# Kernel optimization log

Hardware: AMD Instinct MI355X
Metric: run time of the kernel (lower is better)

## Reference

```python
import jax, jax.numpy as jnp
import numpy as np

B, C, H, W = 2, 3, 96, 96
OC = 2  # conv output channels
EPS = 1e-5

def setup_inputs() -> dict:
    key = jax.random.key(0)
    k1, k2, k3, k4 = jax.random.split(key, 4)
    return {
        "X_tnext": jax.random.normal(k1, (B, C, H, W), dtype=jnp.float32),
        "X_hat_tnext": jax.random.normal(k2, (B, C, H, W), dtype=jnp.float32),
        "conv_w": jax.random.normal(k3, (OC, C, 3, 3), dtype=jnp.float32) * 0.1,
        "conv_b": jax.random.normal(k4, (OC,), dtype=jnp.float32) * 0.1,
        "gamma": jnp.ones((OC,), dtype=jnp.float32),
        "beta": jnp.zeros((OC,), dtype=jnp.float32),
    }

def reference(X_tnext, X_hat_tnext, conv_w, conv_b, gamma, beta):
    b, c, h, w = X_tnext.shape
    n = h * w
    q = X_tnext.reshape(b, c, n)
    k = X_hat_tnext.reshape(b, c, n)
    # corr4D: [b, n, n] = q^T k / sqrt(c)  (materialized O(N^2) volume, as in source)
    corr = jnp.einsum('bcn,bcm->bnm', q, k) / jnp.sqrt(jnp.asarray(c, jnp.float32))
    # weighted aggregation: corr @ X_tnext (broadcast over channels)
    agg = jnp.einsum('bnm,bcm->bcn', corr, q).reshape(b, c, h, w)
    # Conv2d(3->2, k=3, s=1, p=1)
    y = jax.lax.conv_general_dilated(
        agg, conv_w, window_strides=(1, 1), padding='SAME',
        dimension_numbers=('NCHW', 'OIHW', 'NCHW'))
    y = y + conv_b[None, :, None, None]
    # BatchNorm2d (training-mode batch statistics, biased var, eps=1e-5)
    mean = jnp.mean(y, axis=(0, 2, 3), keepdims=True)
    var = jnp.var(y, axis=(0, 2, 3), keepdims=True)
    y = (y - mean) * jax.lax.rsqrt(var + EPS)
    y = y * gamma[None, :, None, None] + beta[None, :, None, None]
    # LeakyReLU(0.1)
    return jnp.where(y >= 0, y, 0.1 * y)
```

## Files before the change

kernel.cpp:

```cpp
#include <hip/hip_runtime.h>
#include <math.h>

namespace {
constexpr int kB = 2, kC = 3, kOC = 2, kH = 96, kW = 96;
constexpr int kN   = kH * kW;
constexpr int kPix = kB * kOC * kN;
constexpr float kEps   = 1e-5f;
constexpr float kScale = 0.57735026918962576f;

constexpr int WS_M   = 0;
constexpr int WS_SUM = 24;
constexpr int WS_SQ  = 26;
constexpr int WS_Y   = 32;
}

__global__ void k1_corr(const float* __restrict__ q, const float* __restrict__ kk,
                        float* __restrict__ ws) {
    const int idx = blockIdx.x;
    const int b   = idx / 9;
    const int cp  = (idx % 9) / 3;
    const int c   = idx % 3;
    const float* kp = kk + (size_t)(b * kC + cp) * kN;
    const float* qp = q  + (size_t)(b * kC + c ) * kN;
    float part = 0.f;
    for (int n = threadIdx.x; n < kN; n += 256)
        part += kp[n] * qp[n];
    __shared__ float red[256];
    red[threadIdx.x] = part;
    __syncthreads();
    for (int s = 128; s > 0; s >>= 1) {
        if (threadIdx.x < s) red[threadIdx.x] += red[threadIdx.x + s];
        __syncthreads();
    }
    if (threadIdx.x == 0) {
        ws[WS_M + idx] = red[0];
        if (idx == 0) {
            ws[WS_SUM + 0] = 0.f; ws[WS_SUM + 1] = 0.f;
            ws[WS_SQ  + 0] = 0.f; ws[WS_SQ  + 1] = 0.f;
        }
    }
}

__global__ void k2_conv(const float* __restrict__ q, const float* __restrict__ cw,
                        const float* __restrict__ cb, float* __restrict__ ws) {
    const int plane = blockIdx.x / 36;
    const int b   = plane / kOC;
    const int oc  = plane % kOC;
    const int pix = (blockIdx.x % 36) * 256 + threadIdx.x;
    const int h = pix / kW, w = pix % kW;

    __shared__ float sM[9];
    __shared__ float sW[kC * 9];
    if (threadIdx.x < 9) sM[threadIdx.x] = ws[WS_M + b * 9 + threadIdx.x];
    if (threadIdx.x >= 64 && threadIdx.x < 64 + kC * 9)
        sW[threadIdx.x - 64] = cw[oc * kC * 9 + (threadIdx.x - 64)];
    __syncthreads();

    const float* qb = q + (size_t)b * kC * kN;
    float acc = cb[oc];
    #pragma unroll
    for (int dh = 0; dh < 3; ++dh) {
        const int hh = h + dh - 1;
        if (hh < 0 || hh >= kH) continue;
        #pragma unroll
        for (int dw = 0; dw < 3; ++dw) {
            const int ww = w + dw - 1;
            if (ww < 0 || ww >= kW) continue;
            const int p = hh * kW + ww;
            const float q0 = qb[p];
            const float q1 = qb[kN + p];
            const float q2 = qb[2 * kN + p];
            #pragma unroll
            for (int ic = 0; ic < kC; ++ic) {
                const float a = kScale * (sM[0 * 3 + ic] * q0 +
                                          sM[1 * 3 + ic] * q1 +
                                          sM[2 * 3 + ic] * q2);
                acc += a * sW[ic * 9 + dh * 3 + dw];
            }
        }
    }
    ws[WS_Y + plane * kN + pix] = acc;

    __shared__ float rs[256], rq[256];
    rs[threadIdx.x] = acc;
    rq[threadIdx.x] = acc * acc;
    __syncthreads();
    for (int s = 128; s > 0; s >>= 1) {
        if (threadIdx.x < s) {
            rs[threadIdx.x] += rs[threadIdx.x + s];
            rq[threadIdx.x] += rq[threadIdx.x + s];
        }
        __syncthreads();
    }
    if (threadIdx.x == 0) {
        atomicAdd(&ws[WS_SUM + oc], rs[0]);
        atomicAdd(&ws[WS_SQ  + oc], rq[0]);
    }
}

__global__ void k3_bn(const float* __restrict__ ws, const float* __restrict__ gamma,
                      const float* __restrict__ beta, float* __restrict__ out) {
    const int i  = blockIdx.x * 256 + threadIdx.x;
    const int oc = (i / kN) % kOC;
    const float inv  = 1.f / (float)(kB * kN);
    const float mean = ws[WS_SUM + oc] * inv;
    const float var  = ws[WS_SQ + oc] * inv - mean * mean;
    const float rstd = rsqrtf(var + kEps);
    float y = (ws[WS_Y + i] - mean) * rstd * gamma[oc] + beta[oc];
    out[i] = (y >= 0.f) ? y : 0.1f * y;
}

extern "C" void kernel_launch(void* const* d_in, const int* in_sizes, int n_in,
                              void* d_out, int out_size, void* d_ws, size_t ws_size,
                              hipStream_t stream) {
    const float* X      = (const float*)d_in[0];
    const float* Xhat   = (const float*)d_in[1];
    const float* conv_w = (const float*)d_in[2];
    const float* conv_b = (const float*)d_in[3];
    const float* gamma  = (const float*)d_in[4];
    const float* beta   = (const float*)d_in[5];
    float* out = (float*)d_out;
    float* ws  = (float*)d_ws;

    k1_corr<<<kB * kC * kC, 256, 0, stream>>>(X, Xhat, ws);
    k2_conv<<<kPix / 256, 256, 0, stream>>>(X, conv_w, conv_b, ws);
    k3_bn  <<<kPix / 256, 256, 0, stream>>>(ws, gamma, beta, out);
}
```

Baseline: 83.04 us.

## Fuse correlation, conv and batchnorm into one kernel with grid barrier

Merges the three kernels into one launch. Each block recomputes the 3x3 channel correlation matrix itself, using warp shuffles instead of a separate reduction kernel, then runs the convolution. Blocks publish per-block partial sums and spin on a global atomic counter until all have arrived, then reduce the batchnorm statistics and write the output directly, so the intermediate Y buffer is never written or re-read. The barrier assumes all 144 blocks are resident at once. It also relies on the workspace counter being set to a poison value before each call so the first block can reset it, which depends on harness behaviour. Every block also repeats the correlation reads, trading redundant work for fewer launches.

```diff
diff --git a/kernel.cpp b/kernel.cpp
--- a/kernel.cpp
+++ b/kernel.cpp
@@ -3,60 +3,64 @@
 
 namespace {
 constexpr int kB = 2, kC = 3, kOC = 2, kH = 96, kW = 96;
-constexpr int kN   = kH * kW;
-constexpr int kPix = kB * kOC * kN;
+constexpr int kN      = kH * kW;
+constexpr int kChunks = kN / 256;
+constexpr int kBlocks = kB * kOC * kChunks;
 constexpr float kEps   = 1e-5f;
 constexpr float kScale = 0.57735026918962576f;
-
-constexpr int WS_M   = 0;
-constexpr int WS_SUM = 24;
-constexpr int WS_SQ  = 26;
-constexpr int WS_Y   = 32;
+constexpr unsigned kPoison = 0xAAAAAAAAu;
 }
 
-__global__ void k1_corr(const float* __restrict__ q, const float* __restrict__ kk,
-                        float* __restrict__ ws) {
-    const int idx = blockIdx.x;
-    const int b   = idx / 9;
-    const int cp  = (idx % 9) / 3;
-    const int c   = idx % 3;
-    const float* kp = kk + (size_t)(b * kC + cp) * kN;
-    const float* qp = q  + (size_t)(b * kC + c ) * kN;
-    float part = 0.f;
-    for (int n = threadIdx.x; n < kN; n += 256)
-        part += kp[n] * qp[n];
-    __shared__ float red[256];
-    red[threadIdx.x] = part;
-    __syncthreads();
-    for (int s = 128; s > 0; s >>= 1) {
-        if (threadIdx.x < s) red[threadIdx.x] += red[threadIdx.x + s];
-        __syncthreads();
-    }
-    if (threadIdx.x == 0) {
-        ws[WS_M + idx] = red[0];
-        if (idx == 0) {
-            ws[WS_SUM + 0] = 0.f; ws[WS_SUM + 1] = 0.f;
-            ws[WS_SQ  + 0] = 0.f; ws[WS_SQ  + 1] = 0.f;
-        }
-    }
-}
+__global__ __launch_bounds__(256) void fused_fea(
+    const float* __restrict__ X,    const float* __restrict__ Xhat,
+    const float* __restrict__ cw,   const float* __restrict__ cb,
+    const float* __restrict__ gamma,const float* __restrict__ beta,
+    float* __restrict__ out, unsigned* __restrict__ wsu) {
 
-__global__ void k2_conv(const float* __restrict__ q, const float* __restrict__ cw,
-                        const float* __restrict__ cb, float* __restrict__ ws) {
-    const int plane = blockIdx.x / 36;
-    const int b   = plane / kOC;
-    const int oc  = plane % kOC;
-    const int pix = (blockIdx.x % 36) * 256 + threadIdx.x;
+    const int tid   = threadIdx.x;
+    const int blk   = blockIdx.x;
+    const int plane = blk / kChunks;
+    const int b     = plane / kOC;
+    const int oc    = plane % kOC;
+    const int pix   = (blk % kChunks) * 256 + tid;
     const int h = pix / kW, w = pix % kW;
 
+    float* wsf = (float*)wsu;
+
     __shared__ float sM[9];
+    __shared__ float sMw[4][9];
     __shared__ float sW[kC * 9];
-    if (threadIdx.x < 9) sM[threadIdx.x] = ws[WS_M + b * 9 + threadIdx.x];
-    if (threadIdx.x >= 64 && threadIdx.x < 64 + kC * 9)
-        sW[threadIdx.x - 64] = cw[oc * kC * 9 + (threadIdx.x - 64)];
+    __shared__ float sRed[256], sRed2[256];
+    __shared__ float sStats[2];
+
+    if (tid >= 32 && tid < 32 + kC * 9) sW[tid - 32] = cw[oc * kC * 9 + (tid - 32)];
+
+    const float* qb = X    + (size_t)b * kC * kN;
+    const float* kb = Xhat + (size_t)b * kC * kN;
+    float m0=0,m1=0,m2=0,m3=0,m4=0,m5=0,m6=0,m7=0,m8=0;
+    for (int n = tid; n < kN; n += 256) {
+        float q0 = qb[n], q1 = qb[kN + n], q2 = qb[2 * kN + n];
+        float k0 = kb[n], k1 = kb[kN + n], k2 = kb[2 * kN + n];
+        m0 += k0 * q0; m1 += k0 * q1; m2 += k0 * q2;
+        m3 += k1 * q0; m4 += k1 * q1; m5 += k1 * q2;
+        m6 += k2 * q0; m7 += k2 * q1; m8 += k2 * q2;
+    }
+    #pragma unroll
+    for (int off = 32; off > 0; off >>= 1) {
+        m0 += __shfl_down(m0, off); m1 += __shfl_down(m1, off); m2 += __shfl_down(m2, off);
+        m3 += __shfl_down(m3, off); m4 += __shfl_down(m4, off); m5 += __shfl_down(m5, off);
+        m6 += __shfl_down(m6, off); m7 += __shfl_down(m7, off); m8 += __shfl_down(m8, off);
+    }
+    const int wave = tid >> 6;
+    if ((tid & 63) == 0) {
+        sMw[wave][0]=m0; sMw[wave][1]=m1; sMw[wave][2]=m2;
+        sMw[wave][3]=m3; sMw[wave][4]=m4; sMw[wave][5]=m5;
+        sMw[wave][6]=m6; sMw[wave][7]=m7; sMw[wave][8]=m8;
+    }
+    __syncthreads();
+    if (tid < 9) sM[tid] = sMw[0][tid] + sMw[1][tid] + sMw[2][tid] + sMw[3][tid];
     __syncthreads();
 
-    const float* qb = q + (size_t)b * kC * kN;
     float acc = cb[oc];
     #pragma unroll
     for (int dh = 0; dh < 3; ++dh) {
@@ -79,35 +83,54 @@
             }
         }
     }
-    ws[WS_Y + plane * kN + pix] = acc;
 
-    __shared__ float rs[256], rq[256];
-    rs[threadIdx.x] = acc;
-    rq[threadIdx.x] = acc * acc;
+    sRed[tid]  = acc;
+    sRed2[tid] = acc * acc;
     __syncthreads();
     for (int s = 128; s > 0; s >>= 1) {
-        if (threadIdx.x < s) {
-            rs[threadIdx.x] += rs[threadIdx.x + s];
-            rq[threadIdx.x] += rq[threadIdx.x + s];
-        }
+        if (tid < s) { sRed[tid] += sRed[tid + s]; sRed2[tid] += sRed2[tid + s]; }
         __syncthreads();
     }
-    if (threadIdx.x == 0) {
-        atomicAdd(&ws[WS_SUM + oc], rs[0]);
-        atomicAdd(&ws[WS_SQ  + oc], rq[0]);
+
+    if (tid == 0) {
+        __hip_atomic_store(&wsf[8 + blk * 2 + 0], sRed[0],  __ATOMIC_RELAXED, __HIP_MEMORY_SCOPE_AGENT);
+        __hip_atomic_store(&wsf[8 + blk * 2 + 1], sRed2[0], __ATOMIC_RELAXED, __HIP_MEMORY_SCOPE_AGENT);
+        unsigned expected = kPoison;
+        __hip_atomic_compare_exchange_strong(&wsu[0], &expected, 0u,
+            __ATOMIC_RELAXED, __ATOMIC_RELAXED, __HIP_MEMORY_SCOPE_AGENT);
+        __hip_atomic_fetch_add(&wsu[0], 1u, __ATOMIC_RELEASE, __HIP_MEMORY_SCOPE_AGENT);
+        while (__hip_atomic_load(&wsu[0], __ATOMIC_ACQUIRE, __HIP_MEMORY_SCOPE_AGENT)
+               < (unsigned)kBlocks) {
+            __builtin_amdgcn_s_sleep(1);
+        }
     }
-}
+    __syncthreads();
 
-__global__ void k3_bn(const float* __restrict__ ws, const float* __restrict__ gamma,
-                      const float* __restrict__ beta, float* __restrict__ out) {
-    const int i  = blockIdx.x * 256 + threadIdx.x;
-    const int oc = (i / kN) % kOC;
-    const float inv  = 1.f / (float)(kB * kN);
-    const float mean = ws[WS_SUM + oc] * inv;
-    const float var  = ws[WS_SQ + oc] * inv - mean * mean;
-    const float rstd = rsqrtf(var + kEps);
-    float y = (ws[WS_Y + i] - mean) * rstd * gamma[oc] + beta[oc];
-    out[i] = (y >= 0.f) ? y : 0.1f * y;
+    float ps = 0.f, pq = 0.f;
+    if (tid < 2 * kChunks) {
+        const int j = (tid < kChunks) ? (oc * kChunks + tid)
+                                      : ((kOC + oc) * kChunks + (tid - kChunks));
+        ps = __hip_atomic_load(&wsf[8 + j * 2 + 0], __ATOMIC_RELAXED, __HIP_MEMORY_SCOPE_AGENT);
+        pq = __hip_atomic_load(&wsf[8 + j * 2 + 1], __ATOMIC_RELAXED, __HIP_MEMORY_SCOPE_AGENT);
+    }
+    sRed[tid]  = (tid < 2 * kChunks) ? ps : 0.f;
+    sRed2[tid] = (tid < 2 * kChunks) ? pq : 0.f;
+    __syncthreads();
+    for (int s = 128; s > 0; s >>= 1) {
+        if (tid < s) { sRed[tid] += sRed[tid + s]; sRed2[tid] += sRed2[tid + s]; }
+        __syncthreads();
+    }
+    if (tid == 0) {
+        const float inv  = 1.f / (float)(kB * kN);
+        const float mean = sRed[0] * inv;
+        const float var  = sRed2[0] * inv - mean * mean;
+        sStats[0] = mean;
+        sStats[1] = rsqrtf(var + kEps);
+    }
+    __syncthreads();
+
+    float y = (acc - sStats[0]) * sStats[1] * gamma[oc] + beta[oc];
+    out[plane * kN + pix] = (y >= 0.f) ? y : 0.1f * y;
 }
 
 extern "C" void kernel_launch(void* const* d_in, const int* in_sizes, int n_in,
@@ -119,10 +142,7 @@
     const float* conv_b = (const float*)d_in[3];
     const float* gamma  = (const float*)d_in[4];
     const float* beta   = (const float*)d_in[5];
-    float* out = (float*)d_out;
-    float* ws  = (float*)d_ws;
 
-    k1_corr<<<kB * kC * kC, 256, 0, stream>>>(X, Xhat, ws);
-    k2_conv<<<kPix / 256, 256, 0, stream>>>(X, conv_w, conv_b, ws);
-    k3_bn  <<<kPix / 256, 256, 0, stream>>>(ws, gamma, beta, out);
+    fused_fea<<<kBlocks, 256, 0, stream>>>(X, Xhat, conv_w, conv_b, gamma, beta,
+                                           (float*)d_out, (unsigned*)d_ws);
 }
```

Result: slower. 88.10 us (+6.1%).

## Fold Gram matrix into conv weights, compute both output channels per thread, drop atomics

Applied to the files above, without the earlier changes.

Precomputes effective conv weights by folding the 3x3 Gram matrix and scale into the conv filter. Each thread now computes both output channels, which halves the conv grid and reuses the input loads. Per-block partial statistics are written to the workspace instead of atomically accumulated, and the BN kernel reduces them itself, so the zeroing step and the atomics go away. Reductions use wavefront shuffles and the Gram kernel uses float4 loads. The cost is that every BN block redundantly reduces the 72 partials.

```diff
diff --git a/kernel.cpp b/kernel.cpp
--- a/kernel.cpp
+++ b/kernel.cpp
@@ -3,61 +3,59 @@
 
 namespace {
 constexpr int kB = 2, kC = 3, kOC = 2, kH = 96, kW = 96;
-constexpr int kN   = kH * kW;
-constexpr int kPix = kB * kOC * kN;
+constexpr int kN      = kH * kW;
+constexpr int kChunks = kN / 256;
 constexpr float kEps   = 1e-5f;
 constexpr float kScale = 0.57735026918962576f;
-
-constexpr int WS_M   = 0;
-constexpr int WS_SUM = 24;
-constexpr int WS_SQ  = 26;
-constexpr int WS_Y   = 32;
+constexpr int WS_M = 0;
+constexpr int WS_P = 32;
+constexpr int WS_Y = 512;
 }
 
-__global__ void k1_corr(const float* __restrict__ q, const float* __restrict__ kk,
-                        float* __restrict__ ws) {
+__global__ __launch_bounds__(256) void k1_gram(const float* __restrict__ X,
+                                               const float* __restrict__ Xh,
+                                               float* __restrict__ ws) {
     const int idx = blockIdx.x;
-    const int b   = idx / 9;
-    const int cp  = (idx % 9) / 3;
-    const int c   = idx % 3;
-    const float* kp = kk + (size_t)(b * kC + cp) * kN;
-    const float* qp = q  + (size_t)(b * kC + c ) * kN;
+    const int b = idx / 9, cp = (idx % 9) / 3, c = idx % 3;
+    const float4* kp = (const float4*)(Xh + (size_t)(b * kC + cp) * kN);
+    const float4* qp = (const float4*)(X  + (size_t)(b * kC + c ) * kN);
     float part = 0.f;
-    for (int n = threadIdx.x; n < kN; n += 256)
-        part += kp[n] * qp[n];
-    __shared__ float red[256];
-    red[threadIdx.x] = part;
+    for (int n = threadIdx.x; n < kN / 4; n += 256) {
+        const float4 a = kp[n], q = qp[n];
+        part += a.x * q.x + a.y * q.y + a.z * q.z + a.w * q.w;
+    }
+    #pragma unroll
+    for (int off = 32; off > 0; off >>= 1) part += __shfl_down(part, off);
+    __shared__ float sw[4];
+    if ((threadIdx.x & 63) == 0) sw[threadIdx.x >> 6] = part;
     __syncthreads();
-    for (int s = 128; s > 0; s >>= 1) {
-        if (threadIdx.x < s) red[threadIdx.x] += red[threadIdx.x + s];
-        __syncthreads();
-    }
-    if (threadIdx.x == 0) {
-        ws[WS_M + idx] = red[0];
-        if (idx == 0) {
-            ws[WS_SUM + 0] = 0.f; ws[WS_SUM + 1] = 0.f;
-            ws[WS_SQ  + 0] = 0.f; ws[WS_SQ  + 1] = 0.f;
-        }
-    }
+    if (threadIdx.x == 0) ws[WS_M + idx] = sw[0] + sw[1] + sw[2] + sw[3];
 }
 
-__global__ void k2_conv(const float* __restrict__ q, const float* __restrict__ cw,
-                        const float* __restrict__ cb, float* __restrict__ ws) {
-    const int plane = blockIdx.x / 36;
-    const int b   = plane / kOC;
-    const int oc  = plane % kOC;
-    const int pix = (blockIdx.x % 36) * 256 + threadIdx.x;
+__global__ __launch_bounds__(256) void k2_conv(const float* __restrict__ X,
+                                               const float* __restrict__ cw,
+                                               const float* __restrict__ cb,
+                                               float* __restrict__ ws) {
+    const int tid = threadIdx.x;
+    const int blk = blockIdx.x;
+    const int b   = blk / kChunks;
+    const int pix = (blk % kChunks) * 256 + tid;
     const int h = pix / kW, w = pix % kW;
 
     __shared__ float sM[9];
-    __shared__ float sW[kC * 9];
-    if (threadIdx.x < 9) sM[threadIdx.x] = ws[WS_M + b * 9 + threadIdx.x];
-    if (threadIdx.x >= 64 && threadIdx.x < 64 + kC * 9)
-        sW[threadIdx.x - 64] = cw[oc * kC * 9 + (threadIdx.x - 64)];
+    __shared__ float sE[2][3][9];
+    if (tid < 9) sM[tid] = ws[WS_M + b * 9 + tid];
+    __syncthreads();
+    if (tid < 54) {
+        const int oc = tid / 27, r = tid % 27, cp = r / 9, nb = r % 9;
+        sE[oc][cp][nb] = kScale * (cw[oc * 27 +      nb] * sM[cp * 3 + 0] +
+                                   cw[oc * 27 +  9 + nb] * sM[cp * 3 + 1] +
+                                   cw[oc * 27 + 18 + nb] * sM[cp * 3 + 2]);
+    }
     __syncthreads();
 
-    const float* qb = q + (size_t)b * kC * kN;
-    float acc = cb[oc];
+    const float* qb = X + (size_t)b * kC * kN;
+    float acc0 = cb[0], acc1 = cb[1];
     #pragma unroll
     for (int dh = 0; dh < 3; ++dh) {
         const int hh = h + dh - 1;
@@ -66,47 +64,57 @@
         for (int dw = 0; dw < 3; ++dw) {
             const int ww = w + dw - 1;
             if (ww < 0 || ww >= kW) continue;
-            const int p = hh * kW + ww;
-            const float q0 = qb[p];
-            const float q1 = qb[kN + p];
-            const float q2 = qb[2 * kN + p];
-            #pragma unroll
-            for (int ic = 0; ic < kC; ++ic) {
-                const float a = kScale * (sM[0 * 3 + ic] * q0 +
-                                          sM[1 * 3 + ic] * q1 +
-                                          sM[2 * 3 + ic] * q2);
-                acc += a * sW[ic * 9 + dh * 3 + dw];
-            }
+            const int p = hh * kW + ww, nb = dh * 3 + dw;
+            const float q0 = qb[p], q1 = qb[kN + p], q2 = qb[2 * kN + p];
+            acc0 += q0 * sE[0][0][nb] + q1 * sE[0][1][nb] + q2 * sE[0][2][nb];
+            acc1 += q0 * sE[1][0][nb] + q1 * sE[1][1][nb] + q2 * sE[1][2][nb];
         }
     }
-    ws[WS_Y + plane * kN + pix] = acc;
+    ws[WS_Y + (b * kOC + 0) * kN + pix] = acc0;
+    ws[WS_Y + (b * kOC + 1) * kN + pix] = acc1;
 
-    __shared__ float rs[256], rq[256];
-    rs[threadIdx.x] = acc;
-    rq[threadIdx.x] = acc * acc;
+    float v0 = acc0, v1 = acc0 * acc0, v2 = acc1, v3 = acc1 * acc1;
+    #pragma unroll
+    for (int off = 32; off > 0; off >>= 1) {
+        v0 += __shfl_down(v0, off); v1 += __shfl_down(v1, off);
+        v2 += __shfl_down(v2, off); v3 += __shfl_down(v3, off);
+    }
+    __shared__ float sP[4][4];
+    if ((tid & 63) == 0) {
+        const int wv = tid >> 6;
+        sP[wv][0] = v0; sP[wv][1] = v1; sP[wv][2] = v2; sP[wv][3] = v3;
+    }
     __syncthreads();
-    for (int s = 128; s > 0; s >>= 1) {
-        if (threadIdx.x < s) {
-            rs[threadIdx.x] += rs[threadIdx.x + s];
-            rq[threadIdx.x] += rq[threadIdx.x + s];
+    if (tid < 4) ws[WS_P + blk * 4 + tid] = sP[0][tid] + sP[1][tid] + sP[2][tid] + sP[3][tid];
+}
+
+__global__ __launch_bounds__(256) void k3_bn(const float* __restrict__ ws,
+                                             const float* __restrict__ gamma,
+                                             const float* __restrict__ beta,
+                                             float* __restrict__ out) {
+    const int tid = threadIdx.x;
+    const int i   = blockIdx.x * 256 + tid;
+    const int oc  = (i / kN) & 1;
+    __shared__ float sS[128], sQ[128];
+    if (tid < 128) {
+        float s = 0.f, q = 0.f;
+        if (tid < 72) {
+            s = ws[WS_P + tid * 4 + oc * 2];
+            q = ws[WS_P + tid * 4 + oc * 2 + 1];
         }
+        sS[tid] = s; sQ[tid] = q;
+    }
+    __syncthreads();
+    for (int st = 64; st > 0; st >>= 1) {
+        if (tid < st) { sS[tid] += sS[tid + st]; sQ[tid] += sQ[tid + st]; }
         __syncthreads();
     }
-    if (threadIdx.x == 0) {
-        atomicAdd(&ws[WS_SUM + oc], rs[0]);
-        atomicAdd(&ws[WS_SQ  + oc], rq[0]);
-    }
-}
-
-__global__ void k3_bn(const float* __restrict__ ws, const float* __restrict__ gamma,
-                      const float* __restrict__ beta, float* __restrict__ out) {
-    const int i  = blockIdx.x * 256 + threadIdx.x;
-    const int oc = (i / kN) % kOC;
     const float inv  = 1.f / (float)(kB * kN);
-    const float mean = ws[WS_SUM + oc] * inv;
-    const float var  = ws[WS_SQ + oc] * inv - mean * mean;
-    const float rstd = rsqrtf(var + kEps);
-    float y = (ws[WS_Y + i] - mean) * rstd * gamma[oc] + beta[oc];
+    const float mean = sS[0] * inv;
+    const float var  = sQ[0] * inv - mean * mean;
+    const float g    = gamma[oc] * rsqrtf(var + kEps);
+    const float bt   = beta[oc];
+    const float y = (ws[WS_Y + i] - mean) * g + bt;
     out[i] = (y >= 0.f) ? y : 0.1f * y;
 }
 
@@ -119,10 +127,9 @@
     const float* conv_b = (const float*)d_in[3];
     const float* gamma  = (const float*)d_in[4];
     const float* beta   = (const float*)d_in[5];
-    float* out = (float*)d_out;
     float* ws  = (float*)d_ws;
 
-    k1_corr<<<kB * kC * kC, 256, 0, stream>>>(X, Xhat, ws);
-    k2_conv<<<kPix / 256, 256, 0, stream>>>(X, conv_w, conv_b, ws);
-    k3_bn  <<<kPix / 256, 256, 0, stream>>>(ws, gamma, beta, out);
+    k1_gram<<<kB * 9, 256, 0, stream>>>(X, Xhat, ws);
+    k2_conv<<<kB * kChunks, 256, 0, stream>>>(X, conv_w, conv_b, ws);
+    k3_bn  <<<kB * kOC * kChunks, 256, 0, stream>>>(ws, gamma, beta, (float*)d_out);
 }
```

Measured after the change: 73.60 us. 1.13x faster.
